# Kernel optimization log

Measured on AMD Instinct MI355X. Metric: run time of the kernel, lower is better.

## Reference

```python
import jax, jax.numpy as jnp
import numpy as np

T, B, E, H, O = 128, 512, 256, 1024, 256


def setup_inputs() -> dict:
    key = jax.random.key(0)
    ks = jax.random.split(key, 7)
    s = lambda k, shape, fan: jax.random.normal(k, shape, jnp.float32) / np.sqrt(fan)
    return {
        "seq": jax.random.normal(ks[0], (T, B, E), jnp.float32),
        "Wh_w": s(ks[1], (H, H), H),
        "Wh_b": s(ks[2], (H,), H),
        "Wi_w": s(ks[3], (H, E), E),
        "Wi_b": s(ks[4], (H,), E),
        "Wo_w": s(ks[5], (O, H), H),
        "Wo_b": s(ks[6], (O,), H),
    }


def reference(seq, Wh_w, Wh_b, Wi_w, Wi_b, Wo_w, Wo_b):
    # Elman RNN: h_t = tanh(Wh h_{t-1} + Wi x_t); returns o_T = Wo h_T.
    Bsz = seq.shape[1]
    h0 = jnp.zeros((Bsz, Wh_w.shape[0]), seq.dtype)
    # Precompute input projections for all steps in one big GEMM: [T,B,H]
    xi = jnp.einsum('tbe,he->tbh', seq, Wi_w) + Wi_b + Wh_b

    def step(h, xt):
        h = jnp.tanh(h @ Wh_w.T + xt)
        return h, None

    hT, _ = jax.lax.scan(step, h0, xi)
    return hT @ Wo_w.T + Wo_b
```

## Files before the change

kernel.cpp:

```cpp
#include <hip/hip_runtime.h>
#include <hip/hip_bf16.h>


#define T_ 128
#define B_ 512
#define E_ 256
#define H_ 1024
#define O_ 256
#define RG 16
#define HB (B_ * H_)

typedef __bf16 bf16x8 __attribute__((ext_vector_type(8)));
typedef float  f32x4  __attribute__((ext_vector_type(4)));
typedef unsigned int u32x2 __attribute__((ext_vector_type(2)));
typedef unsigned int u32x4 __attribute__((ext_vector_type(4)));

static __device__ __forceinline__ unsigned short f2bf(float f) {
  unsigned u = __float_as_uint(f);
  u += 0x7fff + ((u >> 16) & 1);
  return (unsigned short)(u >> 16);
}
static __device__ __forceinline__ unsigned pk2(float a, float b) {
  return (unsigned)f2bf(a) | ((unsigned)f2bf(b) << 16);
}
static __device__ __forceinline__ bf16x8 cvt8(const float* p) {
  float4 f0 = reinterpret_cast<const float4*>(p)[0];
  float4 f1 = reinterpret_cast<const float4*>(p)[1];
  union { u32x4 u; bf16x8 v; } r;
  r.u = (u32x4){pk2(f0.x, f0.y), pk2(f0.z, f0.w), pk2(f1.x, f1.y), pk2(f1.z, f1.w)};
  return r.v;
}
static __device__ __forceinline__ float fast_tanh(float x) {
  float e = __builtin_amdgcn_exp2f(x * 2.8853900817779268f);
  return 1.f - 2.f / (e + 1.f);
}

static __device__ __forceinline__ void poll1(const unsigned* fl, unsigned tgt) {
  for (;;) {
    unsigned a;
    asm volatile("global_load_dword %0, %1, off sc0 sc1"
                 : "=v"(a) : "v"(fl) : "memory");
    asm volatile("s_waitcnt vmcnt(0)" ::: "memory");
    __builtin_amdgcn_sched_barrier(0);
    if (a >= tgt) return;
    __builtin_amdgcn_s_sleep(1);
  }
}

__global__ void prep_kernel(const float* __restrict__ seq,
                            unsigned short* __restrict__ seq_bf,
                            unsigned* __restrict__ flags) {
  size_t idx = (size_t)blockIdx.x * blockDim.x + threadIdx.x;
  size_t stride = (size_t)gridDim.x * blockDim.x;
  const size_t nchunk = (size_t)T_ * B_ * E_ / 8;
  for (size_t i = idx; i < nchunk; i += stride) {
    union { bf16x8 v; u32x4 u; } r;
    r.v = cvt8(seq + i * 8);
    *reinterpret_cast<u32x4*>(seq_bf + i * 8) = r.u;
  }
  if (idx < 8192) {
    unsigned z = 0;
    asm volatile("global_store_dword %0, %1, off sc0 sc1"
                 :: "v"(flags + idx), "v"(z) : "memory");
  }
}

__global__ __launch_bounds__(512, 2) void rnn_fused(
    const unsigned short* __restrict__ seq_bf, const float* __restrict__ Wh_w,
    const float* __restrict__ Wh_b, const float* __restrict__ Wi_w,
    const float* __restrict__ Wi_b, const float* __restrict__ Wo_w,
    const float* __restrict__ Wo_b,
    unsigned short* __restrict__ hbuf, unsigned* __restrict__ flags,
    float* __restrict__ out) {
  __shared__ __align__(16) float red[8][RG][132];

  const int tid = threadIdx.x;
  const int bid = blockIdx.x;
  const int g = bid & 31, p = bid >> 5;
  const int R0 = g * RG, C0 = p * 128;
  const int lane = tid & 63, wv = tid >> 6;
  const int l15 = lane & 15, k4 = lane >> 4;

  bf16x8 bh[8][4];
#pragma unroll
  for (int nn = 0; nn < 8; ++nn) {
    const float* wp = Wh_w + (size_t)(C0 + nn * 16 + l15) * H_ + wv * 128 + k4 * 8;
#pragma unroll
    for (int ks = 0; ks < 4; ++ks) bh[nn][ks] = cvt8(wp + ks * 32);
  }
  bf16x8 wif[8];
#pragma unroll
  for (int nn = 0; nn < 8; ++nn)
    wif[nn] = cvt8(Wi_w + (size_t)(C0 + nn * 16 + l15) * E_ + wv * 32 + k4 * 8);

  const int erow = tid >> 5, ec = (tid & 31) * 4;
  f32x4 bias4;
  {
    f32x4 b1 = *reinterpret_cast<const f32x4*>(Wh_b + C0 + ec);
    f32x4 b2 = *reinterpret_cast<const f32x4*>(Wi_b + C0 + ec);
    bias4 = b1 + b2;
  }
  const unsigned* wvfl = flags + g * 256 + wv * 32;
  unsigned* myfl = flags + g * 256 + p * 32;
  const size_t hoff_b = ((size_t)(R0 + erow) * H_ + C0 + ec) * 2;
  const size_t afr_b = (size_t)(R0 + l15) * 2048 + wv * 256 + k4 * 16;

  for (int t = 0; t < T_; ++t) {
    f32x4 acc[8];
#pragma unroll
    for (int nn = 0; nn < 8; ++nn) acc[nn] = (f32x4){0.f, 0.f, 0.f, 0.f};
    union { u32x4 u; bf16x8 v; } xa;
    {
      const unsigned char* xp = (const unsigned char*)seq_bf +
          (((size_t)t * B_ + R0 + l15) * E_ + wv * 32 + k4 * 8) * 2;
      asm volatile("global_load_dwordx4 %0, %1, off"
                   : "=v"(xa.u) : "v"(xp) : "memory");
    }
    u32x4 a0, a1, a2, a3;
    if (t > 0) {
      poll1(wvfl, (unsigned)t);
      const unsigned char* ab =
          (const unsigned char*)hbuf + (size_t)((t - 1) & 1) * (HB * 2) + afr_b;
      asm volatile("global_load_dwordx4 %0, %1, off sc0 sc1"
                   : "=v"(a0) : "v"(ab) : "memory");
      asm volatile("global_load_dwordx4 %0, %1, off sc0 sc1"
                   : "=v"(a1) : "v"(ab + 64) : "memory");
      asm volatile("global_load_dwordx4 %0, %1, off sc0 sc1"
                   : "=v"(a2) : "v"(ab + 128) : "memory");
      asm volatile("global_load_dwordx4 %0, %1, off sc0 sc1"
                   : "=v"(a3) : "v"(ab + 192) : "memory");
    } else {
      asm volatile("s_waitcnt vmcnt(0)" ::: "memory");
      __builtin_amdgcn_sched_barrier(0);
    }
#pragma unroll
    for (int nn = 0; nn < 8; ++nn)
      acc[nn] = __builtin_amdgcn_mfma_f32_16x16x32_bf16(xa.v, wif[nn], acc[nn], 0, 0, 0);
    if (t > 0) {
      union { u32x4 u; bf16x8 v; } af;
#define RNN_HMF(N, KS, AV)                                                       \
      asm volatile("s_waitcnt vmcnt(" #N ")" ::: "memory");                      \
      __builtin_amdgcn_sched_barrier(0);                           \
      af.u = AV;                                                                 \
      _Pragma("unroll")                                                          \
      for (int nn = 0; nn < 8; ++nn)                                             \
        acc[nn] = __builtin_amdgcn_mfma_f32_16x16x32_bf16(af.v, bh[nn][KS],      \
                                                          acc[nn], 0, 0, 0);
      RNN_HMF(3, 0, a0) RNN_HMF(2, 1, a1) RNN_HMF(1, 2, a2) RNN_HMF(0, 3, a3)
#undef RNN_HMF
    }
#pragma unroll
    for (int nn = 0; nn < 8; ++nn)
#pragma unroll
      for (int r = 0; r < 4; ++r)
        red[wv][k4 * 4 + r][nn * 16 + l15] = acc[nn][r];
    __syncthreads();
    {
      f32x4 v = *reinterpret_cast<const f32x4*>(&red[0][erow][ec]);
#pragma unroll
      for (int s = 1; s < 8; ++s)
        v += *reinterpret_cast<const f32x4*>(&red[s][erow][ec]);
      v += bias4;
      u32x2 pv = {pk2(fast_tanh(v[0]), fast_tanh(v[1])),
                  pk2(fast_tanh(v[2]), fast_tanh(v[3]))};
      const unsigned char* dst =
          (const unsigned char*)hbuf + (size_t)(t & 1) * (HB * 2) + hoff_b;
      asm volatile("global_store_dwordx2 %0, %1, off sc0 sc1"
                   :: "v"(dst), "v"(pv) : "memory");
    }
    asm volatile("s_waitcnt vmcnt(0)" ::: "memory");
    __syncthreads();
    if (tid == 0) {
      unsigned fv = (unsigned)(t + 1);
      asm volatile("global_store_dword %0, %1, off sc0 sc1"
                   :: "v"(myfl), "v"(fv) : "memory");
    }
  }

  if (p >= 2) return;
  {
    poll1(wvfl, (unsigned)T_);
    const unsigned char* ab =
        (const unsigned char*)hbuf + (size_t)((T_ - 1) & 1) * (HB * 2) + afr_b;
    u32x4 a0, a1, a2, a3;
    asm volatile("global_load_dwordx4 %0, %1, off sc0 sc1" : "=v"(a0) : "v"(ab) : "memory");
    asm volatile("global_load_dwordx4 %0, %1, off sc0 sc1" : "=v"(a1) : "v"(ab + 64) : "memory");
    asm volatile("global_load_dwordx4 %0, %1, off sc0 sc1" : "=v"(a2) : "v"(ab + 128) : "memory");
    asm volatile("global_load_dwordx4 %0, %1, off sc0 sc1" : "=v"(a3) : "v"(ab + 192) : "memory");
    asm volatile("s_waitcnt vmcnt(0)" ::: "memory");
    __builtin_amdgcn_sched_barrier(0);
    f32x4 acc[8];
#pragma unroll
    for (int nn = 0; nn < 8; ++nn) acc[nn] = (f32x4){0.f, 0.f, 0.f, 0.f};
    union { u32x4 u; bf16x8 v; } af;
#define RNN_OMF(KS, AV)                                                          \
    af.u = AV;                                                                   \
    _Pragma("unroll")                                                            \
    for (int nn = 0; nn < 8; ++nn) {                                             \
      bf16x8 b = cvt8(Wo_w + (size_t)(C0 + nn * 16 + l15) * H_ +                 \
                      wv * 128 + (KS) * 32 + k4 * 8);                            \
      acc[nn] = __builtin_amdgcn_mfma_f32_16x16x32_bf16(af.v, b, acc[nn], 0, 0, 0); \
    }
    RNN_OMF(0, a0) RNN_OMF(1, a1) RNN_OMF(2, a2) RNN_OMF(3, a3)
#undef RNN_OMF
#pragma unroll
    for (int nn = 0; nn < 8; ++nn)
#pragma unroll
      for (int r = 0; r < 4; ++r)
        red[wv][k4 * 4 + r][nn * 16 + l15] = acc[nn][r];
    __syncthreads();
    {
      f32x4 v = *reinterpret_cast<const f32x4*>(&red[0][erow][ec]);
#pragma unroll
      for (int s = 1; s < 8; ++s)
        v += *reinterpret_cast<const f32x4*>(&red[s][erow][ec]);
      v += *reinterpret_cast<const f32x4*>(Wo_b + C0 + ec);
      *reinterpret_cast<f32x4*>(out + (size_t)(R0 + erow) * O_ + C0 + ec) = v;
    }
  }
}

extern "C" void kernel_launch(void* const* d_in, const int* in_sizes, int n_in,
                              void* d_out, int out_size, void* d_ws, size_t ws_size,
                              hipStream_t stream) {
  const float* seq  = (const float*)d_in[0];
  const float* Wh_w = (const float*)d_in[1];
  const float* Wh_b = (const float*)d_in[2];
  const float* Wi_w = (const float*)d_in[3];
  const float* Wi_b = (const float*)d_in[4];
  const float* Wo_w = (const float*)d_in[5];
  const float* Wo_b = (const float*)d_in[6];

  char* ws = (char*)d_ws;
  unsigned short* hbuf   = (unsigned short*)ws; ws += (size_t)2 * HB * 2;
  unsigned*       flags  = (unsigned*)ws;       ws += 32768;
  unsigned short* seq_bf = (unsigned short*)ws;

  prep_kernel<<<2048, 256, 0, stream>>>(seq, seq_bf, flags);
  rnn_fused<<<256, 512, 0, stream>>>(seq_bf, Wh_w, Wh_b, Wi_w, Wi_b, Wo_w, Wo_b,
                                     hbuf, flags, (float*)d_out);
}
```

Baseline: 405.8 us.

## Use per-wave completion flags and double-buffered LDS to drop block barrier

Each wave now publishes its own progress flag after storing its part of h_t, instead of a block-wide __syncthreads followed by a single flag store. Consumers poll the eight producer-wave flags covering their K slice and take the minimum. The LDS reduction buffer is double-buffered by step parity, which lets the trailing block barrier be removed safely. The aim is to cut intra-block sync latency on the recurrent critical path, at the cost of eight flag loads per poll and a larger flag area.

```diff
diff --git a/kernel.cpp b/kernel.cpp
--- a/kernel.cpp
+++ b/kernel.cpp
@@ -35,14 +35,22 @@
   return 1.f - 2.f / (e + 1.f);
 }
 
-static __device__ __forceinline__ void poll1(const unsigned* fl, unsigned tgt) {
+static __device__ __forceinline__ void poll8L(const unsigned* fl, unsigned tgt) {
   for (;;) {
-    unsigned a;
-    asm volatile("global_load_dword %0, %1, off sc0 sc1"
-                 : "=v"(a) : "v"(fl) : "memory");
+    unsigned f0, f1, f2, f3, f4, f5, f6, f7;
+    asm volatile("global_load_dword %0, %1, off sc0 sc1" : "=v"(f0) : "v"(fl) : "memory");
+    asm volatile("global_load_dword %0, %1, off sc0 sc1" : "=v"(f1) : "v"(fl + 32) : "memory");
+    asm volatile("global_load_dword %0, %1, off sc0 sc1" : "=v"(f2) : "v"(fl + 64) : "memory");
+    asm volatile("global_load_dword %0, %1, off sc0 sc1" : "=v"(f3) : "v"(fl + 96) : "memory");
+    asm volatile("global_load_dword %0, %1, off sc0 sc1" : "=v"(f4) : "v"(fl + 128) : "memory");
+    asm volatile("global_load_dword %0, %1, off sc0 sc1" : "=v"(f5) : "v"(fl + 160) : "memory");
+    asm volatile("global_load_dword %0, %1, off sc0 sc1" : "=v"(f6) : "v"(fl + 192) : "memory");
+    asm volatile("global_load_dword %0, %1, off sc0 sc1" : "=v"(f7) : "v"(fl + 224) : "memory");
     asm volatile("s_waitcnt vmcnt(0)" ::: "memory");
     __builtin_amdgcn_sched_barrier(0);
-    if (a >= tgt) return;
+    unsigned m = min(min(min(f0, f1), min(f2, f3)),
+                     min(min(f4, f5), min(f6, f7)));
+    if (m >= tgt) return;
     __builtin_amdgcn_s_sleep(1);
   }
 }
@@ -58,7 +66,7 @@
     r.v = cvt8(seq + i * 8);
     *reinterpret_cast<u32x4*>(seq_bf + i * 8) = r.u;
   }
-  if (idx < 8192) {
+  if (idx < 65536) {
     unsigned z = 0;
     asm volatile("global_store_dword %0, %1, off sc0 sc1"
                  :: "v"(flags + idx), "v"(z) : "memory");
@@ -72,7 +80,7 @@
     const float* __restrict__ Wo_b,
     unsigned short* __restrict__ hbuf, unsigned* __restrict__ flags,
     float* __restrict__ out) {
-  __shared__ __align__(16) float red[8][RG][132];
+  __shared__ __align__(16) float red[2][8][RG][132];
 
   const int tid = threadIdx.x;
   const int bid = blockIdx.x;
@@ -100,8 +108,8 @@
     f32x4 b2 = *reinterpret_cast<const f32x4*>(Wi_b + C0 + ec);
     bias4 = b1 + b2;
   }
-  const unsigned* wvfl = flags + g * 256 + wv * 32;
-  unsigned* myfl = flags + g * 256 + p * 32;
+  const unsigned* wvfl = flags + (size_t)(g * 64 + wv * 8) * 32;
+  unsigned* myfl = flags + (size_t)(g * 64 + p * 8 + wv) * 32;
   const size_t hoff_b = ((size_t)(R0 + erow) * H_ + C0 + ec) * 2;
   const size_t afr_b = (size_t)(R0 + l15) * 2048 + wv * 256 + k4 * 16;
 
@@ -118,7 +126,7 @@
     }
     u32x4 a0, a1, a2, a3;
     if (t > 0) {
-      poll1(wvfl, (unsigned)t);
+      poll8L(wvfl, (unsigned)t);
       const unsigned char* ab =
           (const unsigned char*)hbuf + (size_t)((t - 1) & 1) * (HB * 2) + afr_b;
       asm volatile("global_load_dwordx4 %0, %1, off sc0 sc1"
@@ -153,13 +161,13 @@
     for (int nn = 0; nn < 8; ++nn)
 #pragma unroll
       for (int r = 0; r < 4; ++r)
-        red[wv][k4 * 4 + r][nn * 16 + l15] = acc[nn][r];
+        red[t & 1][wv][k4 * 4 + r][nn * 16 + l15] = acc[nn][r];
     __syncthreads();
     {
-      f32x4 v = *reinterpret_cast<const f32x4*>(&red[0][erow][ec]);
+      f32x4 v = *reinterpret_cast<const f32x4*>(&red[t & 1][0][erow][ec]);
 #pragma unroll
       for (int s = 1; s < 8; ++s)
-        v += *reinterpret_cast<const f32x4*>(&red[s][erow][ec]);
+        v += *reinterpret_cast<const f32x4*>(&red[t & 1][s][erow][ec]);
       v += bias4;
       u32x2 pv = {pk2(fast_tanh(v[0]), fast_tanh(v[1])),
                   pk2(fast_tanh(v[2]), fast_tanh(v[3]))};
@@ -169,8 +177,7 @@
                    :: "v"(dst), "v"(pv) : "memory");
     }
     asm volatile("s_waitcnt vmcnt(0)" ::: "memory");
-    __syncthreads();
-    if (tid == 0) {
+    if (lane == 0) {
       unsigned fv = (unsigned)(t + 1);
       asm volatile("global_store_dword %0, %1, off sc0 sc1"
                    :: "v"(myfl), "v"(fv) : "memory");
@@ -179,7 +186,7 @@
 
   if (p >= 2) return;
   {
-    poll1(wvfl, (unsigned)T_);
+    poll8L(wvfl, (unsigned)T_);
     const unsigned char* ab =
         (const unsigned char*)hbuf + (size_t)((T_ - 1) & 1) * (HB * 2) + afr_b;
     u32x4 a0, a1, a2, a3;
@@ -207,13 +214,13 @@
     for (int nn = 0; nn < 8; ++nn)
 #pragma unroll
       for (int r = 0; r < 4; ++r)
-        red[wv][k4 * 4 + r][nn * 16 + l15] = acc[nn][r];
+        red[0][wv][k4 * 4 + r][nn * 16 + l15] = acc[nn][r];
     __syncthreads();
     {
-      f32x4 v = *reinterpret_cast<const f32x4*>(&red[0][erow][ec]);
+      f32x4 v = *reinterpret_cast<const f32x4*>(&red[0][0][erow][ec]);
 #pragma unroll
       for (int s = 1; s < 8; ++s)
-        v += *reinterpret_cast<const f32x4*>(&red[s][erow][ec]);
+        v += *reinterpret_cast<const f32x4*>(&red[0][s][erow][ec]);
       v += *reinterpret_cast<const f32x4*>(Wo_b + C0 + ec);
       *reinterpret_cast<f32x4*>(out + (size_t)(R0 + erow) * O_ + C0 + ec) = v;
     }
@@ -233,7 +240,7 @@
 
   char* ws = (char*)d_ws;
   unsigned short* hbuf   = (unsigned short*)ws; ws += (size_t)2 * HB * 2;
-  unsigned*       flags  = (unsigned*)ws;       ws += 32768;
+  unsigned*       flags  = (unsigned*)ws;       ws += 262144;
   unsigned short* seq_bf = (unsigned short*)ws;
 
   prep_kernel<<<2048, 256, 0, stream>>>(seq, seq_bf, flags);
```

Result: slower. 499.5 us (+23.1%).

## Double-buffer reduction LDS and signal step completion via per-wave LDS counter

Applied to the files above, without the earlier changes.

The LDS reduction buffer is double-buffered by timestep parity. This removes the second block-wide barrier and the full vmcnt(0) drain that used to come before publishing the step flag. Each wave now waits only for its own h store, then increments an LDS counter, and the eighth wave publishes the global flag. The next step's input load is also prefetched across the step boundary. In exchange, LDS use doubles to about 135KB per block, which rules out two blocks per CU, and correctness now rests on subtler ordering between waves.

```diff
diff --git a/kernel.cpp b/kernel.cpp
--- a/kernel.cpp
+++ b/kernel.cpp
@@ -72,7 +72,8 @@
     const float* __restrict__ Wo_b,
     unsigned short* __restrict__ hbuf, unsigned* __restrict__ flags,
     float* __restrict__ out) {
-  __shared__ __align__(16) float red[8][RG][132];
+  __shared__ __align__(16) float red[2][8][RG][132];
+  __shared__ unsigned cnt[2];
 
   const int tid = threadIdx.x;
   const int bid = blockIdx.x;
@@ -81,6 +82,8 @@
   const int lane = tid & 63, wv = tid >> 6;
   const int l15 = lane & 15, k4 = lane >> 4;
 
+  if (tid == 0) { cnt[0] = 0; cnt[1] = 0; }
+
   bf16x8 bh[8][4];
 #pragma unroll
   for (int nn = 0; nn < 8; ++nn) {
@@ -104,18 +107,17 @@
   unsigned* myfl = flags + g * 256 + p * 32;
   const size_t hoff_b = ((size_t)(R0 + erow) * H_ + C0 + ec) * 2;
   const size_t afr_b = (size_t)(R0 + l15) * 2048 + wv * 256 + k4 * 16;
+  const unsigned char* xp0 = (const unsigned char*)seq_bf +
+      (((size_t)R0 + l15) * E_ + wv * 32 + k4 * 8) * 2;
+
+  union { u32x4 u; bf16x8 v; } xa;
+  asm volatile("global_load_dwordx4 %0, %1, off"
+               : "=v"(xa.u) : "v"(xp0) : "memory");
 
   for (int t = 0; t < T_; ++t) {
     f32x4 acc[8];
 #pragma unroll
     for (int nn = 0; nn < 8; ++nn) acc[nn] = (f32x4){0.f, 0.f, 0.f, 0.f};
-    union { u32x4 u; bf16x8 v; } xa;
-    {
-      const unsigned char* xp = (const unsigned char*)seq_bf +
-          (((size_t)t * B_ + R0 + l15) * E_ + wv * 32 + k4 * 8) * 2;
-      asm volatile("global_load_dwordx4 %0, %1, off"
-                   : "=v"(xa.u) : "v"(xp) : "memory");
-    }
     u32x4 a0, a1, a2, a3;
     if (t > 0) {
       poll1(wvfl, (unsigned)t);
@@ -153,13 +155,13 @@
     for (int nn = 0; nn < 8; ++nn)
 #pragma unroll
       for (int r = 0; r < 4; ++r)
-        red[wv][k4 * 4 + r][nn * 16 + l15] = acc[nn][r];
+        red[t & 1][wv][k4 * 4 + r][nn * 16 + l15] = acc[nn][r];
     __syncthreads();
     {
-      f32x4 v = *reinterpret_cast<const f32x4*>(&red[0][erow][ec]);
+      f32x4 v = *reinterpret_cast<const f32x4*>(&red[t & 1][0][erow][ec]);
 #pragma unroll
       for (int s = 1; s < 8; ++s)
-        v += *reinterpret_cast<const f32x4*>(&red[s][erow][ec]);
+        v += *reinterpret_cast<const f32x4*>(&red[t & 1][s][erow][ec]);
       v += bias4;
       u32x2 pv = {pk2(fast_tanh(v[0]), fast_tanh(v[1])),
                   pk2(fast_tanh(v[2]), fast_tanh(v[3]))};
@@ -168,12 +170,21 @@
       asm volatile("global_store_dwordx2 %0, %1, off sc0 sc1"
                    :: "v"(dst), "v"(pv) : "memory");
     }
-    asm volatile("s_waitcnt vmcnt(0)" ::: "memory");
-    __syncthreads();
-    if (tid == 0) {
-      unsigned fv = (unsigned)(t + 1);
-      asm volatile("global_store_dword %0, %1, off sc0 sc1"
-                   :: "v"(myfl), "v"(fv) : "memory");
+    {
+      int tn = (t + 1 < T_) ? (t + 1) : t;
+      const unsigned char* xp = xp0 + (size_t)tn * (B_ * E_ * 2);
+      asm volatile("global_load_dwordx4 %0, %1, off"
+                   : "=v"(xa.u) : "v"(xp) : "memory");
+    }
+    asm volatile("s_waitcnt vmcnt(1)" ::: "memory");
+    if (lane == 0) {
+      unsigned old = atomicAdd(&cnt[t & 1], 1u);
+      if (old == 7u) {
+        unsigned fv = (unsigned)(t + 1);
+        asm volatile("global_store_dword %0, %1, off sc0 sc1"
+                     :: "v"(myfl), "v"(fv) : "memory");
+        cnt[t & 1] = 0;
+      }
     }
   }
 
@@ -207,13 +218,13 @@
     for (int nn = 0; nn < 8; ++nn)
 #pragma unroll
       for (int r = 0; r < 4; ++r)
-        red[wv][k4 * 4 + r][nn * 16 + l15] = acc[nn][r];
+        red[0][wv][k4 * 4 + r][nn * 16 + l15] = acc[nn][r];
     __syncthreads();
     {
-      f32x4 v = *reinterpret_cast<const f32x4*>(&red[0][erow][ec]);
+      f32x4 v = *reinterpret_cast<const f32x4*>(&red[0][0][erow][ec]);
 #pragma unroll
       for (int s = 1; s < 8; ++s)
-        v += *reinterpret_cast<const f32x4*>(&red[s][erow][ec]);
+        v += *reinterpret_cast<const f32x4*>(&red[0][s][erow][ec]);
       v += *reinterpret_cast<const f32x4*>(Wo_b + C0 + ec);
       *reinterpret_cast<f32x4*>(out + (size_t)(R0 + erow) * O_ + C0 + ec) = v;
     }
```

Measured after the change: 420.4 us. 1.04x slower.
